# Kernel tuning notes

Hardware: AMD Instinct MI355X
Metric: run time of the kernel (lower is better)

The kernel has to match this reference:

```python
import jax, jax.numpy as jnp
import numpy as np

H = 8          # num_heads
WIN = 63       # win_size
LEFT = WIN - 1 - WIN // 2  # 31
EPS = 1e-5


def layer_norm(x, w, b):
    mu = x.mean(-1, keepdims=True)
    var = ((x - mu) ** 2).mean(-1, keepdims=True)
    return (x - mu) / jnp.sqrt(var + EPS) * w + b


def setup_inputs() -> dict:
    key = jax.random.key(0)
    N, T, C = 2, 2048, 512
    hid = 4 * C
    ks = jax.random.split(key, 16)
    s = 0.02
    return {
        "x": jax.random.normal(ks[0], (N, T, C), jnp.float32),
        "norm1_w": jnp.ones((C,), jnp.float32),
        "norm1_b": jnp.zeros((C,), jnp.float32),
        "qkv_w": jax.random.normal(ks[1], (3 * C, C), jnp.float32) * s,
        "qkv_b": jnp.zeros((3 * C,), jnp.float32),
        "rel_bias": jax.random.normal(ks[2], (H, WIN), jnp.float32) * s,
        "proj_w": jax.random.normal(ks[3], (C, C), jnp.float32) * s,
        "proj_b": jnp.zeros((C,), jnp.float32),
        "norm2_w": jnp.ones((C,), jnp.float32),
        "norm2_b": jnp.zeros((C,), jnp.float32),
        "fc1_w": jax.random.normal(ks[4], (hid, C), jnp.float32) * s,
        "fc1_b": jnp.zeros((hid,), jnp.float32),
        "fc2_w": jax.random.normal(ks[5], (C, hid), jnp.float32) * s,
        "fc2_b": jnp.zeros((C,), jnp.float32),
    }


def reference(x, norm1_w, norm1_b, qkv_w, qkv_b, rel_bias, proj_w, proj_b,
              norm2_w, norm2_b, fc1_w, fc1_b, fc2_w, fc2_b):
    N, T, C = x.shape
    hd = C // H
    scale = hd ** -0.5
    right = WIN - LEFT - 1

    shortcut = x
    h = layer_norm(x, norm1_w, norm1_b)
    qkv = (h @ qkv_w.T + qkv_b).reshape(N, T, 3, H, hd)
    q, k, v = qkv[:, :, 0], qkv[:, :, 1], qkv[:, :, 2]  # (N,T,H,hd)

    # zero-pad keys/values along time, gather sliding windows
    kp = jnp.pad(k, ((0, 0), (LEFT, right), (0, 0), (0, 0)))
    vp = jnp.pad(v, ((0, 0), (LEFT, right), (0, 0), (0, 0)))
    idx = jnp.arange(T)[:, None] + jnp.arange(WIN)[None, :]
    k_win = kp[:, idx]
    v_win = vp[:, idx]

    attn = jnp.einsum('nthd,ntwhd->nhtw', q * scale, k_win)
    attn = attn + rel_bias[None, :, None, :]
    # boundary mask: key position j = t - LEFT + w must lie in [0, T)
    pos = idx - LEFT
    mask = jnp.where((pos < 0) | (pos >= T), jnp.float32(-100.0), jnp.float32(0.0))
    attn = attn + mask[None, None, :, :]
    attn = jax.nn.softmax(attn, axis=-1)

    out = jnp.einsum('nhtw,ntwhd->nthd', attn, v_win).reshape(N, T, C)
    out = out @ proj_w.T + proj_b

    x = shortcut + out
    h2 = layer_norm(x, norm2_w, norm2_b)
    m = jax.nn.gelu(h2 @ fc1_w.T + fc1_b, approximate=False)  # torch nn.GELU = exact erf
    m = m @ fc2_w.T + fc2_b
    return x + m
```

## Files before the change

kernel.cpp:

```cpp
#include <hip/hip_runtime.h>

typedef unsigned short u16;
typedef unsigned int uint;
typedef __attribute__((ext_vector_type(4))) float floatx4;
typedef __attribute__((ext_vector_type(16))) float floatx16;
typedef __attribute__((ext_vector_type(8))) short shortx8;

__device__ __forceinline__ u16 f2b(float f) {
    unsigned int u = __float_as_uint(f);
    unsigned int r = (u + 0x7fffu + ((u >> 16) & 1u)) >> 16;
    return (u16)r;
}
__device__ __forceinline__ float b2f(u16 u) {
    return __uint_as_float(((unsigned int)u) << 16);
}
__device__ __forceinline__ void gl_lds16(const u16* g, u16* l) {
    __builtin_amdgcn_global_load_lds(
        (const __attribute__((address_space(1))) void*)g,
        (__attribute__((address_space(3))) void*)l, 16, 0, 0);
}
__device__ __forceinline__ float gelu_f(float v) {
    float e = __expf(1.59576912f * v * (1.0f + 0.044715f * v * v));
    return v * e / (e + 1.0f);
}
__device__ __forceinline__ void cvt_block(const float* __restrict__ src,
                                          u16* __restrict__ dst, int i0) {
    int i = i0 * 256 + threadIdx.x;
    float4 v = ((const float4*)src)[i];
    uint2 o;
    o.x = (uint)f2b(v.x) | ((uint)f2b(v.y) << 16);
    o.y = (uint)f2b(v.z) | ((uint)f2b(v.w) << 16);
    ((uint2*)dst)[i] = o;
}

__device__ __forceinline__ void ln_row_wave_f32(const float* __restrict__ x,
                                                const float* __restrict__ w,
                                                const float* __restrict__ b,
                                                u16* __restrict__ out, int row) {
    int lane = threadIdx.x & 63;
    const float4* xr = (const float4*)(x + (size_t)row * 512);
    float4 v0 = xr[lane * 2], v1 = xr[lane * 2 + 1];
    float s = v0.x + v0.y + v0.z + v0.w + v1.x + v1.y + v1.z + v1.w;
    float s2 = v0.x * v0.x + v0.y * v0.y + v0.z * v0.z + v0.w * v0.w +
               v1.x * v1.x + v1.y * v1.y + v1.z * v1.z + v1.w * v1.w;
    #pragma unroll
    for (int o = 32; o > 0; o >>= 1) {
        s += __shfl_xor(s, o, 64);
        s2 += __shfl_xor(s2, o, 64);
    }
    float mu = s * (1.0f / 512.0f);
    float var = s2 * (1.0f / 512.0f) - mu * mu;
    float rstd = rsqrtf(var + 1e-5f);
    const float4* wr = (const float4*)w;
    const float4* br = (const float4*)b;
    float4 w0 = wr[lane * 2], w1 = wr[lane * 2 + 1];
    float4 b0 = br[lane * 2], b1 = br[lane * 2 + 1];
    uint4 o4;
    o4.x = (uint)f2b((v0.x - mu) * rstd * w0.x + b0.x) |
           ((uint)f2b((v0.y - mu) * rstd * w0.y + b0.y) << 16);
    o4.y = (uint)f2b((v0.z - mu) * rstd * w0.z + b0.z) |
           ((uint)f2b((v0.w - mu) * rstd * w0.w + b0.w) << 16);
    o4.z = (uint)f2b((v1.x - mu) * rstd * w1.x + b1.x) |
           ((uint)f2b((v1.y - mu) * rstd * w1.y + b1.y) << 16);
    o4.w = (uint)f2b((v1.z - mu) * rstd * w1.z + b1.z) |
           ((uint)f2b((v1.w - mu) * rstd * w1.w + b1.w) << 16);
    ((uint4*)(out + (size_t)row * 512))[lane] = o4;
}

__global__ __launch_bounds__(256) void ln_kernel_b(const u16* __restrict__ x,
                                                   const float* __restrict__ w,
                                                   const float* __restrict__ b,
                                                   u16* __restrict__ out) {
    int row = blockIdx.x * 4 + (threadIdx.x >> 6);
    int lane = threadIdx.x & 63;
    uint4 p = ((const uint4*)(x + (size_t)row * 512))[lane];
    float v[8];
    v[0] = b2f((u16)(p.x & 0xffffu)); v[1] = b2f((u16)(p.x >> 16));
    v[2] = b2f((u16)(p.y & 0xffffu)); v[3] = b2f((u16)(p.y >> 16));
    v[4] = b2f((u16)(p.z & 0xffffu)); v[5] = b2f((u16)(p.z >> 16));
    v[6] = b2f((u16)(p.w & 0xffffu)); v[7] = b2f((u16)(p.w >> 16));
    float s = 0.f, s2 = 0.f;
    #pragma unroll
    for (int i = 0; i < 8; i++) { s += v[i]; s2 += v[i] * v[i]; }
    #pragma unroll
    for (int o = 32; o > 0; o >>= 1) {
        s += __shfl_xor(s, o, 64);
        s2 += __shfl_xor(s2, o, 64);
    }
    float mu = s * (1.0f / 512.0f);
    float var = s2 * (1.0f / 512.0f) - mu * mu;
    float rstd = rsqrtf(var + 1e-5f);
    const float4* wr = (const float4*)w;
    const float4* br = (const float4*)b;
    float4 w0 = wr[lane * 2], w1 = wr[lane * 2 + 1];
    float4 b0 = br[lane * 2], b1 = br[lane * 2 + 1];
    float o8[8];
    o8[0] = (v[0] - mu) * rstd * w0.x + b0.x;
    o8[1] = (v[1] - mu) * rstd * w0.y + b0.y;
    o8[2] = (v[2] - mu) * rstd * w0.z + b0.z;
    o8[3] = (v[3] - mu) * rstd * w0.w + b0.w;
    o8[4] = (v[4] - mu) * rstd * w1.x + b1.x;
    o8[5] = (v[5] - mu) * rstd * w1.y + b1.y;
    o8[6] = (v[6] - mu) * rstd * w1.z + b1.z;
    o8[7] = (v[7] - mu) * rstd * w1.w + b1.w;
    uint4 o4;
    o4.x = (uint)f2b(o8[0]) | ((uint)f2b(o8[1]) << 16);
    o4.y = (uint)f2b(o8[2]) | ((uint)f2b(o8[3]) << 16);
    o4.z = (uint)f2b(o8[4]) | ((uint)f2b(o8[5]) << 16);
    o4.w = (uint)f2b(o8[6]) | ((uint)f2b(o8[7]) << 16);
    ((uint4*)(out + (size_t)row * 512))[lane] = o4;
}

__global__ __launch_bounds__(256) void prep_kernel(
    const float* __restrict__ qkvw, u16* __restrict__ wq,
    const float* __restrict__ x, const float* __restrict__ n1w,
    const float* __restrict__ n1b, u16* __restrict__ hb) {
    int bi = blockIdx.x;
    if (bi < 768) {
        cvt_block(qkvw, wq, bi);
    } else {
        int row = (bi - 768) * 4 + (threadIdx.x >> 6);
        ln_row_wave_f32(x, n1w, n1b, hb, row);
    }
}

template <int EPI>
__global__ __launch_bounds__(256, 2) void gemm16(const u16* __restrict__ A,
                                                 const u16* __restrict__ W,
                                                 const float* __restrict__ bias,
                                                 u16* __restrict__ outB,
                                                 int M, int Nn, int K, int nby,
                                                 const float* __restrict__ cs0,
                                                 u16* __restrict__ cd0, int cn0,
                                                 const float* __restrict__ cs1,
                                                 u16* __restrict__ cd1, int cn1) {
    constexpr int BM = 128, BN = 128, BK = 64;
    __shared__ u16 a_s[2][BM * BK];
    __shared__ u16 b_s[2][BN * BK];

    if ((int)blockIdx.y >= nby) {
        int flat = ((int)blockIdx.y - nby) * (int)gridDim.x + (int)blockIdx.x;
        if (flat < cn0)            cvt_block(cs0, cd0, flat);
        else if (flat < cn0 + cn1) cvt_block(cs1, cd1, flat - cn0);
        return;
    }

    int tid = threadIdx.x;
    int wid = tid >> 6, lane = tid & 63;
    int wm = wid >> 1, wn = wid & 1;
    int m_blk = blockIdx.x * BM;
    int n_blk = blockIdx.y * BN;
    int lr = lane & 15;
    int lkc = lane >> 4;

    floatx4 acc[4][4];
    #pragma unroll
    for (int i = 0; i < 4; i++)
        #pragma unroll
        for (int j = 0; j < 4; j++) acc[i][j] = (floatx4){0.f, 0.f, 0.f, 0.f};

    const u16* Ag = A + (size_t)m_blk * K;
    const u16* Wg = W + (size_t)n_blk * K;

    int srow = tid >> 3;
    int skc = (tid & 7) ^ (srow & 7);

    auto stage = [&](int k0, int buf) {
        #pragma unroll
        for (int p = 0; p < 4; p++)
            gl_lds16(Ag + (size_t)(p * 32 + srow) * K + k0 + skc * 8,
                     a_s[buf] + (p * 256 + tid) * 8);
        #pragma unroll
        for (int p = 0; p < 4; p++)
            gl_lds16(Wg + (size_t)(p * 32 + srow) * K + k0 + skc * 8,
                     b_s[buf] + (p * 256 + tid) * 8);
    };

    stage(0, 0);
    int nit = K >> 6;
    for (int it = 0; it < nit; it++) {
        __syncthreads();
        if (it + 1 < nit) stage((it + 1) << 6, (it + 1) & 1);
        int cb = it & 1;
        #pragma unroll
        for (int s = 0; s < 2; s++) {
            int kc = s * 4 + lkc;
            shortx8 af[4], bf[4];
            #pragma unroll
            for (int i = 0; i < 4; i++) {
                int row = wm * 64 + i * 16 + lr;
                af[i] = *(const shortx8*)(a_s[cb] + (row * 8 + (kc ^ (row & 7))) * 8);
            }
            #pragma unroll
            for (int j = 0; j < 4; j++) {
                int row = wn * 64 + j * 16 + lr;
                bf[j] = *(const shortx8*)(b_s[cb] + (row * 8 + (kc ^ (row & 7))) * 8);
            }
            #pragma unroll
            for (int i = 0; i < 4; i++)
                #pragma unroll
                for (int j = 0; j < 4; j++)
                    acc[i][j] = __builtin_amdgcn_mfma_f32_16x16x32_bf16(
                        af[i], bf[j], acc[i][j], 0, 0, 0);
        }
    }

    int col_l = lane & 15;
    int row_base = (lane >> 4) * 4;
    #pragma unroll
    for (int nj = 0; nj < 4; nj++) {
        int col = n_blk + wn * 64 + nj * 16 + col_l;
        float bv = bias[col];
        #pragma unroll
        for (int mi = 0; mi < 4; mi++) {
            #pragma unroll
            for (int r = 0; r < 4; r++) {
                int row = m_blk + wm * 64 + mi * 16 + row_base + r;
                size_t off = (size_t)row * Nn + col;
                float v = acc[mi][nj][r] + bv;
                outB[off] = f2b(EPI == 2 ? gelu_f(v) : v);
            }
        }
    }
}

template <int EPI>
__global__ __launch_bounds__(256, 2) void gemm32(const u16* __restrict__ A,
                                                 const u16* __restrict__ W,
                                                 const float* __restrict__ bias,
                                                 const float* __restrict__ residF,
                                                 const u16* __restrict__ residB,
                                                 float* __restrict__ outF,
                                                 u16* __restrict__ outB,
                                                 int M, int Nn, int K) {
    constexpr int BM = 64, BN = 64, BK = 128;
    constexpr int CPR = BK / 8, KMSK = CPR - 1;
    __shared__ u16 a_s[2][BM * BK];
    __shared__ u16 b_s[2][BN * BK];

    int tid = threadIdx.x;
    int wid = tid >> 6, lane = tid & 63;
    int wm = wid >> 1, wn = wid & 1;
    int m_blk = blockIdx.x * BM;
    int n_blk = blockIdx.y * BN;
    int lr = lane & 15;
    int lkc = lane >> 4;

    floatx4 acc[2][2];
    #pragma unroll
    for (int i = 0; i < 2; i++)
        #pragma unroll
        for (int j = 0; j < 2; j++) acc[i][j] = (floatx4){0.f, 0.f, 0.f, 0.f};

    const u16* Ag = A + (size_t)m_blk * K;
    const u16* Wg = W + (size_t)n_blk * K;

    int srow = tid / CPR;
    int skc = (tid & KMSK) ^ (srow & KMSK);

    auto stage = [&](int k0, int buf) {
        #pragma unroll
        for (int p = 0; p < 4; p++)
            gl_lds16(Ag + (size_t)(p * 16 + srow) * K + k0 + skc * 8,
                     a_s[buf] + (p * 256 + tid) * 8);
        #pragma unroll
        for (int p = 0; p < 4; p++)
            gl_lds16(Wg + (size_t)(p * 16 + srow) * K + k0 + skc * 8,
                     b_s[buf] + (p * 256 + tid) * 8);
    };

    stage(0, 0);
    int nit = K / BK;
    for (int it = 0; it < nit; it++) {
        __syncthreads();
        if (it + 1 < nit) stage((it + 1) * BK, (it + 1) & 1);
        int cb = it & 1;
        #pragma unroll
        for (int s = 0; s < 4; s++) {
            int kc = s * 4 + lkc;
            shortx8 af[2], bf[2];
            #pragma unroll
            for (int i = 0; i < 2; i++) {
                int arow = wm * 32 + i * 16 + lr;
                af[i] = *(const shortx8*)(a_s[cb] + (arow * CPR + (kc ^ (arow & KMSK))) * 8);
            }
            #pragma unroll
            for (int j = 0; j < 2; j++) {
                int brow = wn * 32 + j * 16 + lr;
                bf[j] = *(const shortx8*)(b_s[cb] + (brow * CPR + (kc ^ (brow & KMSK))) * 8);
            }
            #pragma unroll
            for (int i = 0; i < 2; i++)
                #pragma unroll
                for (int j = 0; j < 2; j++)
                    acc[i][j] = __builtin_amdgcn_mfma_f32_16x16x32_bf16(
                        af[i], bf[j], acc[i][j], 0, 0, 0);
        }
    }

    int col_l = lane & 15;
    int row_base = (lane >> 4) * 4;
    #pragma unroll
    for (int j = 0; j < 2; j++) {
        int col = n_blk + wn * 32 + j * 16 + col_l;
        float bv = bias[col];
        #pragma unroll
        for (int i = 0; i < 2; i++) {
            #pragma unroll
            for (int r = 0; r < 4; r++) {
                int row = m_blk + wm * 32 + i * 16 + row_base + r;
                size_t off = (size_t)row * Nn + col;
                float v = acc[i][j][r] + bv;
                if (EPI == 1) outB[off] = f2b(v + residF[off]);
                else          outF[off] = v + b2f(residB[off]);
            }
        }
    }
}

__global__ __launch_bounds__(256) void attn_kernel(const u16* __restrict__ qkv,
                                                   const float* __restrict__ rel_bias,
                                                   u16* __restrict__ out,
                                                   const float* __restrict__ csrc,
                                                   u16* __restrict__ cdst) {
    __shared__ u16 k_s[128][76];
    __shared__ u16 v_t[64][154];
    __shared__ u16 p_s[4][16][106];
    __shared__ float s_bias[64];

    int bx = blockIdx.x;
    if (bx >= 512) {
        cvt_block(csrc, cdst, bx - 512);
        return;
    }
    int n = bx >> 8;
    int h = (bx >> 5) & 7;
    int t0 = (bx & 31) << 6;
    int tid = threadIdx.x, wid = tid >> 6, lane = tid & 63;
    int col = lane & 15, rq = lane >> 4;

    const u16* qrow = qkv + (size_t)(n * 2048 + t0 + wid * 16 + col) * 1536 + h * 64 + rq * 8;
    shortx8 qf0 = *(const shortx8*)qrow;
    shortx8 qf1 = *(const shortx8*)(qrow + 32);

    if (tid < 63) s_bias[tid] = rel_bias[h * 63 + tid];
    if (tid == 63) s_bias[63] = 0.f;

    const uint* qkv_u = (const uint*)qkv;
    for (int idx = tid; idx < 128 * 16; idx += 256) {
        int row = idx >> 4, j2 = idx & 15;
        int pos = t0 - 31 + row;
        uint2 kv; kv.x = 0u; kv.y = 0u;
        if (pos >= 0 && pos < 2048)
            kv = *(const uint2*)(qkv_u + (size_t)(n * 2048 + pos) * 768 + 256 + h * 32 + j2 * 2);
        *(uint2*)&k_s[row][j2 * 4] = kv;
    }
    for (int idx = tid; idx < 72 * 32; idx += 256) {
        int rp = idx >> 5, j = idx & 31;
        int r0 = rp * 2;
        int p0 = t0 - 31 + r0, p1 = p0 + 1;
        uint a = 0u, b = 0u;
        if (p0 >= 0 && p0 < 2048)
            a = qkv_u[(size_t)(n * 2048 + p0) * 768 + 512 + h * 32 + j];
        if (p1 >= 0 && p1 < 2048)
            b = qkv_u[(size_t)(n * 2048 + p1) * 768 + 512 + h * 32 + j];
        *(uint*)&v_t[2 * j][r0]     = (a & 0xffffu) | (b << 16);
        *(uint*)&v_t[2 * j + 1][r0] = (a >> 16) | (b & 0xffff0000u);
    }
    __syncthreads();

    floatx4 S[5];
    #pragma unroll
    for (int nt = 0; nt < 5; nt++) S[nt] = (floatx4){0.f, 0.f, 0.f, 0.f};
    #pragma unroll
    for (int nt = 0; nt < 5; nt++) {
        const u16* kb = &k_s[wid * 16 + nt * 16 + col][rq * 8];
        shortx8 b0 = *(const shortx8*)kb;
        shortx8 b1 = *(const shortx8*)(kb + 32);
        S[nt] = __builtin_amdgcn_mfma_f32_16x16x32_bf16(qf0, b0, S[nt], 0, 0, 0);
        S[nt] = __builtin_amdgcn_mfma_f32_16x16x32_bf16(qf1, b1, S[nt], 0, 0, 0);
    }

    #pragma unroll
    for (int r = 0; r < 4; r++) {
        int t_row = rq * 4 + r;
        float sc[5];
        float mx = -1e30f;
        #pragma unroll
        for (int nt = 0; nt < 5; nt++) {
            int w = nt * 16 + col - t_row;
            int pos_abs = t0 - 31 + wid * 16 + nt * 16 + col;
            float v;
            if (w < 0 || w > 62) {
                v = -1e30f;
            } else {
                v = S[nt][r] * 0.125f + s_bias[w];
                if (pos_abs < 0 || pos_abs >= 2048) v -= 100.f;
            }
            sc[nt] = v;
            mx = fmaxf(mx, v);
        }
        #pragma unroll
        for (int o = 1; o < 16; o <<= 1) mx = fmaxf(mx, __shfl_xor(mx, o, 64));
        float l = 0.f;
        #pragma unroll
        for (int nt = 0; nt < 5; nt++) {
            sc[nt] = __expf(sc[nt] - mx);
            l += sc[nt];
        }
        #pragma unroll
        for (int o = 1; o < 16; o <<= 1) l += __shfl_xor(l, o, 64);
        float inv = 1.0f / l;
        #pragma unroll
        for (int nt = 0; nt < 5; nt++)
            p_s[wid][t_row][nt * 16 + col] = f2b(sc[nt] * inv);
        p_s[wid][t_row][80 + col] = 0;
    }
    __syncthreads();

    floatx4 O[4];
    #pragma unroll
    for (int dt = 0; dt < 4; dt++) O[dt] = (floatx4){0.f, 0.f, 0.f, 0.f};
    const u16* pr = &p_s[wid][col][rq * 8];
    shortx8 a0 = *(const shortx8*)pr;
    shortx8 a1 = *(const shortx8*)(pr + 32);
    shortx8 a2 = *(const shortx8*)(pr + 64);
    #pragma unroll
    for (int dt = 0; dt < 4; dt++) {
        const u16* vb = &v_t[dt * 16 + col][wid * 16 + rq * 8];
        shortx8 b0 = *(const shortx8*)vb;
        shortx8 b1 = *(const shortx8*)(vb + 32);
        shortx8 b2 = *(const shortx8*)(vb + 64);
        O[dt] = __builtin_amdgcn_mfma_f32_16x16x32_bf16(a0, b0, O[dt], 0, 0, 0);
        O[dt] = __builtin_amdgcn_mfma_f32_16x16x32_bf16(a1, b1, O[dt], 0, 0, 0);
        O[dt] = __builtin_amdgcn_mfma_f32_16x16x32_bf16(a2, b2, O[dt], 0, 0, 0);
    }

    #pragma unroll
    for (int dt = 0; dt < 4; dt++) {
        #pragma unroll
        for (int r = 0; r < 4; r++) {
            int t_row = rq * 4 + r;
            out[(size_t)(n * 2048 + t0 + wid * 16 + t_row) * 512 + h * 64 + dt * 16 + col] =
                f2b(O[dt][r]);
        }
    }
}

extern "C" void kernel_launch(void* const* d_in, const int* in_sizes, int n_in,
                              void* d_out, int out_size, void* d_ws, size_t ws_size,
                              hipStream_t stream) {
    const float* x     = (const float*)d_in[0];
    const float* n1w   = (const float*)d_in[1];
    const float* n1b   = (const float*)d_in[2];
    const float* qkvw  = (const float*)d_in[3];
    const float* qkvbv = (const float*)d_in[4];
    const float* relb  = (const float*)d_in[5];
    const float* projw = (const float*)d_in[6];
    const float* projb = (const float*)d_in[7];
    const float* n2w   = (const float*)d_in[8];
    const float* n2b   = (const float*)d_in[9];
    const float* fc1w  = (const float*)d_in[10];
    const float* fc1b  = (const float*)d_in[11];
    const float* fc2w  = (const float*)d_in[12];
    const float* fc2b  = (const float*)d_in[13];
    float* out = (float*)d_out;

    char* p = (char*)d_ws;
    u16* wq   = (u16*)p;  p += (size_t)786432 * 2;
    u16* wp   = (u16*)p;  p += (size_t)262144 * 2;
    u16* w1   = (u16*)p;  p += (size_t)1048576 * 2;
    u16* w2   = (u16*)p;  p += (size_t)1048576 * 2;
    u16* hb   = (u16*)p;  p += (size_t)2097152 * 2;
    u16* qkvb = (u16*)p;  p += (size_t)6291456 * 2;
    u16* attb = (u16*)p;  p += (size_t)2097152 * 2;
    u16* x2b  = (u16*)p;  p += (size_t)2097152 * 2;
    u16* mb   = (u16*)p;  p += (size_t)8388608 * 2;

    prep_kernel<<<1792, 256, 0, stream>>>(qkvw, wq, x, n1w, n1b, hb);
    gemm16<0><<<dim3(32, 12 + 40), 256, 0, stream>>>(hb, wq, qkvbv, qkvb,
                                                     4096, 1536, 512, 12,
                                                     projw, wp, 256,
                                                     fc1w, w1, 1024);
    attn_kernel<<<512 + 1024, 256, 0, stream>>>(qkvb, relb, attb, fc2w, w2);
    gemm32<1><<<dim3(64, 8), 256, 0, stream>>>(attb, wp, projb, x, nullptr,
                                               nullptr, x2b, 4096, 512, 512);
    ln_kernel_b<<<1024, 256, 0, stream>>>(x2b, n2w, n2b, hb);
    gemm16<2><<<dim3(32, 16), 256, 0, stream>>>(hb, w1, fc1b, mb,
                                                4096, 2048, 512, 16,
                                                nullptr, nullptr, 0,
                                                nullptr, nullptr, 0);
    gemm32<3><<<dim3(64, 8), 256, 0, stream>>>(mb, w2, fc2b, nullptr, x2b,
                                               out, nullptr, 4096, 512, 2048);
}
```

Measured before the change: 164.9 us.

## Fold LayerNorm2 into fc1 GEMM via weight prescaling and row statistics

Removes the standalone LN2 kernel. The LN gain is folded into the fc1 weights, and per-column constants c1 and c2 (W·g and W·b) are precomputed inside the spare blocks of the QKV GEMM. The fc1 GEMM now reads the un-normalized x2 directly. Each block computes per-row mean and rstd for its 128 rows at the start and applies rs*(acc - mu*c1) + c2 + bias in the epilogue. This saves one kernel launch and a write and re-read of the normalized activations, but each of the 16 column blocks recomputes the statistics for its rows, and rounding differs slightly because the un-normalized input is fed to the bf16 MFMA.

```diff
diff --git a/kernel.cpp b/kernel.cpp
--- a/kernel.cpp
+++ b/kernel.cpp
@@ -3,7 +3,6 @@
 typedef unsigned short u16;
 typedef unsigned int uint;
 typedef __attribute__((ext_vector_type(4))) float floatx4;
-typedef __attribute__((ext_vector_type(16))) float floatx16;
 typedef __attribute__((ext_vector_type(8))) short shortx8;
 
 __device__ __forceinline__ u16 f2b(float f) {
@@ -31,6 +30,42 @@
     o.x = (uint)f2b(v.x) | ((uint)f2b(v.y) << 16);
     o.y = (uint)f2b(v.z) | ((uint)f2b(v.w) << 16);
     ((uint2*)dst)[i] = o;
+}
+__device__ __forceinline__ void cvt_fold_block(const float* __restrict__ src,
+                                               const float* __restrict__ g,
+                                               u16* __restrict__ dst, int i0) {
+    int i = i0 * 256 + threadIdx.x;
+    int k = (i * 4) & 511;
+    float4 v = ((const float4*)src)[i];
+    float4 gv = *(const float4*)(g + k);
+    uint2 o;
+    o.x = (uint)f2b(v.x * gv.x) | ((uint)f2b(v.y * gv.y) << 16);
+    o.y = (uint)f2b(v.z * gv.z) | ((uint)f2b(v.w * gv.w) << 16);
+    ((uint2*)dst)[i] = o;
+}
+__device__ __forceinline__ void c1c2_rows(const float* __restrict__ w1src,
+                                          const float* __restrict__ g,
+                                          const float* __restrict__ bb,
+                                          float* __restrict__ c1,
+                                          float* __restrict__ c2, int flat) {
+    int wid = threadIdx.x >> 6, lane = threadIdx.x & 63;
+    int n = flat * 4 + wid;
+    const float4* wr = (const float4*)(w1src + (size_t)n * 512);
+    float4 a0 = wr[lane * 2], a1 = wr[lane * 2 + 1];
+    const float4* gr = (const float4*)g;
+    float4 g0 = gr[lane * 2], g1 = gr[lane * 2 + 1];
+    const float4* br = (const float4*)bb;
+    float4 b0 = br[lane * 2], b1 = br[lane * 2 + 1];
+    float s1 = a0.x * g0.x + a0.y * g0.y + a0.z * g0.z + a0.w * g0.w +
+               a1.x * g1.x + a1.y * g1.y + a1.z * g1.z + a1.w * g1.w;
+    float s2 = a0.x * b0.x + a0.y * b0.y + a0.z * b0.z + a0.w * b0.w +
+               a1.x * b1.x + a1.y * b1.y + a1.z * b1.z + a1.w * b1.w;
+    #pragma unroll
+    for (int o = 32; o > 0; o >>= 1) {
+        s1 += __shfl_xor(s1, o, 64);
+        s2 += __shfl_xor(s2, o, 64);
+    }
+    if (lane == 0) { c1[n] = s1; c2[n] = s2; }
 }
 
 __device__ __forceinline__ void ln_row_wave_f32(const float* __restrict__ x,
@@ -67,50 +102,6 @@
     ((uint4*)(out + (size_t)row * 512))[lane] = o4;
 }
 
-__global__ __launch_bounds__(256) void ln_kernel_b(const u16* __restrict__ x,
-                                                   const float* __restrict__ w,
-                                                   const float* __restrict__ b,
-                                                   u16* __restrict__ out) {
-    int row = blockIdx.x * 4 + (threadIdx.x >> 6);
-    int lane = threadIdx.x & 63;
-    uint4 p = ((const uint4*)(x + (size_t)row * 512))[lane];
-    float v[8];
-    v[0] = b2f((u16)(p.x & 0xffffu)); v[1] = b2f((u16)(p.x >> 16));
-    v[2] = b2f((u16)(p.y & 0xffffu)); v[3] = b2f((u16)(p.y >> 16));
-    v[4] = b2f((u16)(p.z & 0xffffu)); v[5] = b2f((u16)(p.z >> 16));
-    v[6] = b2f((u16)(p.w & 0xffffu)); v[7] = b2f((u16)(p.w >> 16));
-    float s = 0.f, s2 = 0.f;
-    #pragma unroll
-    for (int i = 0; i < 8; i++) { s += v[i]; s2 += v[i] * v[i]; }
-    #pragma unroll
-    for (int o = 32; o > 0; o >>= 1) {
-        s += __shfl_xor(s, o, 64);
-        s2 += __shfl_xor(s2, o, 64);
-    }
-    float mu = s * (1.0f / 512.0f);
-    float var = s2 * (1.0f / 512.0f) - mu * mu;
-    float rstd = rsqrtf(var + 1e-5f);
-    const float4* wr = (const float4*)w;
-    const float4* br = (const float4*)b;
-    float4 w0 = wr[lane * 2], w1 = wr[lane * 2 + 1];
-    float4 b0 = br[lane * 2], b1 = br[lane * 2 + 1];
-    float o8[8];
-    o8[0] = (v[0] - mu) * rstd * w0.x + b0.x;
-    o8[1] = (v[1] - mu) * rstd * w0.y + b0.y;
-    o8[2] = (v[2] - mu) * rstd * w0.z + b0.z;
-    o8[3] = (v[3] - mu) * rstd * w0.w + b0.w;
-    o8[4] = (v[4] - mu) * rstd * w1.x + b1.x;
-    o8[5] = (v[5] - mu) * rstd * w1.y + b1.y;
-    o8[6] = (v[6] - mu) * rstd * w1.z + b1.z;
-    o8[7] = (v[7] - mu) * rstd * w1.w + b1.w;
-    uint4 o4;
-    o4.x = (uint)f2b(o8[0]) | ((uint)f2b(o8[1]) << 16);
-    o4.y = (uint)f2b(o8[2]) | ((uint)f2b(o8[3]) << 16);
-    o4.z = (uint)f2b(o8[4]) | ((uint)f2b(o8[5]) << 16);
-    o4.w = (uint)f2b(o8[6]) | ((uint)f2b(o8[7]) << 16);
-    ((uint4*)(out + (size_t)row * 512))[lane] = o4;
-}
-
 __global__ __launch_bounds__(256) void prep_kernel(
     const float* __restrict__ qkvw, u16* __restrict__ wq,
     const float* __restrict__ x, const float* __restrict__ n1w,
@@ -124,24 +115,31 @@
     }
 }
 
-template <int EPI>
+template <int EPI, int FOLD>
 __global__ __launch_bounds__(256, 2) void gemm16(const u16* __restrict__ A,
                                                  const u16* __restrict__ W,
                                                  const float* __restrict__ bias,
                                                  u16* __restrict__ outB,
                                                  int M, int Nn, int K, int nby,
-                                                 const float* __restrict__ cs0,
-                                                 u16* __restrict__ cd0, int cn0,
-                                                 const float* __restrict__ cs1,
-                                                 u16* __restrict__ cd1, int cn1) {
+                                                 const float* __restrict__ wpsrc,
+                                                 u16* __restrict__ wpdst,
+                                                 const float* __restrict__ w1src,
+                                                 u16* __restrict__ w1dst,
+                                                 const float* __restrict__ g2,
+                                                 const float* __restrict__ b2,
+                                                 float* __restrict__ c1f,
+                                                 float* __restrict__ c2f) {
     constexpr int BM = 128, BN = 128, BK = 64;
     __shared__ u16 a_s[2][BM * BK];
     __shared__ u16 b_s[2][BN * BK];
+    __shared__ float mu_s[128];
+    __shared__ float rs_s[128];
 
     if ((int)blockIdx.y >= nby) {
         int flat = ((int)blockIdx.y - nby) * (int)gridDim.x + (int)blockIdx.x;
-        if (flat < cn0)            cvt_block(cs0, cd0, flat);
-        else if (flat < cn0 + cn1) cvt_block(cs1, cd1, flat - cn0);
+        if (flat < 256)       cvt_block(wpsrc, wpdst, flat);
+        else if (flat < 1280) cvt_fold_block(w1src, g2, w1dst, flat - 256);
+        else if (flat < 1792) c1c2_rows(w1src, g2, b2, c1f, c2f, flat - 1280);
         return;
     }
 
@@ -153,12 +151,6 @@
     int lr = lane & 15;
     int lkc = lane >> 4;
 
-    floatx4 acc[4][4];
-    #pragma unroll
-    for (int i = 0; i < 4; i++)
-        #pragma unroll
-        for (int j = 0; j < 4; j++) acc[i][j] = (floatx4){0.f, 0.f, 0.f, 0.f};
-
     const u16* Ag = A + (size_t)m_blk * K;
     const u16* Wg = W + (size_t)n_blk * K;
 
@@ -177,6 +169,38 @@
     };
 
     stage(0, 0);
+
+    if (FOLD) {
+        int lrow = wid * 32;
+        for (int i = 0; i < 32; ++i) {
+            uint4 pv = ((const uint4*)(A + (size_t)(m_blk + lrow + i) * 512))[lane];
+            float v0 = b2f((u16)(pv.x & 0xffffu)), v1 = b2f((u16)(pv.x >> 16));
+            float v2 = b2f((u16)(pv.y & 0xffffu)), v3 = b2f((u16)(pv.y >> 16));
+            float v4 = b2f((u16)(pv.z & 0xffffu)), v5 = b2f((u16)(pv.z >> 16));
+            float v6 = b2f((u16)(pv.w & 0xffffu)), v7 = b2f((u16)(pv.w >> 16));
+            float s = v0 + v1 + v2 + v3 + v4 + v5 + v6 + v7;
+            float s2 = v0 * v0 + v1 * v1 + v2 * v2 + v3 * v3 +
+                       v4 * v4 + v5 * v5 + v6 * v6 + v7 * v7;
+            #pragma unroll
+            for (int o = 32; o > 0; o >>= 1) {
+                s += __shfl_xor(s, o, 64);
+                s2 += __shfl_xor(s2, o, 64);
+            }
+            float mu = s * (1.0f / 512.0f);
+            float var = s2 * (1.0f / 512.0f) - mu * mu;
+            if (lane == 0) {
+                mu_s[lrow + i] = mu;
+                rs_s[lrow + i] = rsqrtf(var + 1e-5f);
+            }
+        }
+    }
+
+    floatx4 acc[4][4];
+    #pragma unroll
+    for (int i = 0; i < 4; i++)
+        #pragma unroll
+        for (int j = 0; j < 4; j++) acc[i][j] = (floatx4){0.f, 0.f, 0.f, 0.f};
+
     int nit = K >> 6;
     for (int it = 0; it < nit; it++) {
         __syncthreads();
@@ -211,13 +235,20 @@
     for (int nj = 0; nj < 4; nj++) {
         int col = n_blk + wn * 64 + nj * 16 + col_l;
         float bv = bias[col];
+        float c1v = FOLD ? c1f[col] : 0.f;
+        float c2v = FOLD ? c2f[col] : 0.f;
         #pragma unroll
         for (int mi = 0; mi < 4; mi++) {
             #pragma unroll
             for (int r = 0; r < 4; r++) {
-                int row = m_blk + wm * 64 + mi * 16 + row_base + r;
-                size_t off = (size_t)row * Nn + col;
-                float v = acc[mi][nj][r] + bv;
+                int lrow_e = wm * 64 + mi * 16 + row_base + r;
+                size_t off = (size_t)(m_blk + lrow_e) * Nn + col;
+                float v;
+                if (FOLD)
+                    v = rs_s[lrow_e] * (acc[mi][nj][r] - mu_s[lrow_e] * c1v) +
+                        c2v + bv;
+                else
+                    v = acc[mi][nj][r] + bv;
                 outB[off] = f2b(EPI == 2 ? gelu_f(v) : v);
             }
         }
@@ -476,20 +507,19 @@
     u16* attb = (u16*)p;  p += (size_t)2097152 * 2;
     u16* x2b  = (u16*)p;  p += (size_t)2097152 * 2;
     u16* mb   = (u16*)p;  p += (size_t)8388608 * 2;
+    float* c1f = (float*)p; p += (size_t)2048 * 4;
+    float* c2f = (float*)p; p += (size_t)2048 * 4;
 
     prep_kernel<<<1792, 256, 0, stream>>>(qkvw, wq, x, n1w, n1b, hb);
-    gemm16<0><<<dim3(32, 12 + 40), 256, 0, stream>>>(hb, wq, qkvbv, qkvb,
-                                                     4096, 1536, 512, 12,
-                                                     projw, wp, 256,
-                                                     fc1w, w1, 1024);
+    gemm16<0, 0><<<dim3(32, 12 + 56), 256, 0, stream>>>(
+        hb, wq, qkvbv, qkvb, 4096, 1536, 512, 12,
+        projw, wp, fc1w, w1, n2w, n2b, c1f, c2f);
     attn_kernel<<<512 + 1024, 256, 0, stream>>>(qkvb, relb, attb, fc2w, w2);
     gemm32<1><<<dim3(64, 8), 256, 0, stream>>>(attb, wp, projb, x, nullptr,
                                                nullptr, x2b, 4096, 512, 512);
-    ln_kernel_b<<<1024, 256, 0, stream>>>(x2b, n2w, n2b, hb);
-    gemm16<2><<<dim3(32, 16), 256, 0, stream>>>(hb, w1, fc1b, mb,
-                                                4096, 2048, 512, 16,
-                                                nullptr, nullptr, 0,
-                                                nullptr, nullptr, 0);
+    gemm16<2, 1><<<dim3(32, 16), 256, 0, stream>>>(
+        x2b, w1, fc1b, mb, 4096, 2048, 512, 16,
+        nullptr, nullptr, nullptr, nullptr, n2w, n2b, c1f, c2f);
     gemm32<3><<<dim3(64, 8), 256, 0, stream>>>(mb, w2, fc2b, nullptr, x2b,
                                                out, nullptr, 4096, 512, 2048);
 }
```

New measurement: 181.2 us. +9.9%, slower.
